# Optimization experiments

Measured on AMD Instinct MI355X. Metric: run time of the kernel, lower is better.

The kernel has to match this reference:

```python
import jax, jax.numpy as jnp
import numpy as np

N_FFT = 7
HOP = 2
WIN_LEN = 6
N_FREQ = N_FFT // 2 + 1  # onesided -> 4


def setup_inputs() -> dict:
    key = jax.random.key(0)
    k1, k2 = jax.random.split(key)
    x = jax.random.normal(k1, (64, 500000), dtype=jnp.float32)
    w = jax.random.uniform(k2, (WIN_LEN,), dtype=jnp.float32)
    return {"input": x, "window": w}


def reference(input, window):
    # torch.stft(n_fft=7, hop=2, win_length=6, center=False, onesided=True,
    #            normalized=False, return_complex=True)
    B, L = input.shape
    F = 1 + (L - N_FFT) // HOP  # number of frames (center=False)
    # ATen centers a short window inside n_fft zeros: left = (n_fft - win_length) // 2 = 0
    left = (N_FFT - WIN_LEN) // 2
    w_pad = jnp.zeros((N_FFT,), input.dtype).at[left:left + WIN_LEN].set(window)
    # strided framing: idx[f, n] = f*hop + n  -> frames [B, F, n_fft]
    idx = jnp.arange(F)[:, None] * HOP + jnp.arange(N_FFT)[None, :]
    frames = input[:, idx] * w_pad  # [B, F, 7]
    # onesided real DFT as a tiny matmul: exp(-2i*pi*k*n/N) = cos - i*sin
    n = jnp.arange(N_FFT, dtype=input.dtype)
    k = jnp.arange(N_FREQ, dtype=input.dtype)
    ang = (2.0 * np.pi / N_FFT) * n[:, None] * k[None, :]  # [7, 4]
    re = jnp.einsum('bfn,nk->bkf', frames, jnp.cos(ang))   # [B, 4, F]
    im = -jnp.einsum('bfn,nk->bkf', frames, jnp.sin(ang))  # [B, 4, F]
    return jax.lax.complex(re, im)  # complex64 [B, n_freq, n_frames]
```

## Files before the change

kernel.cpp:

```cpp
#include <hip/hip_runtime.h>

#define HOP   2
#define NFFT  7
#define WLEN  6
#define NFREQ 4

__device__ __constant__ const float C7[7] = {
     1.0f,
     0.62348980185873359f,
    -0.22252093395631440f,
    -0.90096886790241915f,
    -0.90096886790241915f,
    -0.22252093395631440f,
     0.62348980185873359f
};
__device__ __constant__ const float S7[7] = {
     0.0f,
     0.78183148246802980f,
     0.97492791218182362f,
     0.43388373911755812f,
    -0.43388373911755812f,
    -0.97492791218182362f,
    -0.78183148246802980f
};

__global__ __launch_bounds__(256) void stft_kernel(
    const float* __restrict__ x, const float* __restrict__ w,
    float* __restrict__ out,
    long long L, long long F, long long HALF, long long in0, long long outn)
{
    const long long f = (long long)blockIdx.x * blockDim.x + threadIdx.x;
    if (f >= F) return;
    const long long b = blockIdx.y;

    const long long xbase = b * L + 2 * f;
    if (xbase + (WLEN - 1) >= in0) return;

    float wx[WLEN];
#pragma unroll
    for (int n = 0; n < WLEN; ++n) {
        wx[n] = x[xbase + n] * w[n];
    }

#pragma unroll
    for (int k = 0; k < NFREQ; ++k) {
        float re = 0.f, im = 0.f;
#pragma unroll
        for (int n = 0; n < WLEN; ++n) {
            const int m = (k * n) % 7;
            re = fmaf(wx[n],  C7[m], re);
            im = fmaf(wx[n], -S7[m], im);
        }
        const long long q = (b * NFREQ + k) * F + f;
        if (q < outn)        out[q] = re;
        if (HALF + q < outn) out[HALF + q] = im;
    }
}

extern "C" void kernel_launch(void* const* d_in, const int* in_sizes, int n_in,
                              void* d_out, int out_size, void* d_ws, size_t ws_size,
                              hipStream_t stream) {
    const float* x = (const float*)d_in[0];
    const float* w = (const float*)d_in[1];
    float* out = (float*)d_out;

    const long long B = 64;
    const long long L = (long long)in_sizes[0] / B;
    const long long F = 1 + (L - NFFT) / HOP;
    const long long HALF = B * NFREQ * F;

    dim3 block(256);
    dim3 grid((unsigned)((F + 255) / 256), (unsigned)B);
    stft_kernel<<<grid, block, 0, stream>>>(x, w, out, L, F, HALF,
                                            (long long)in_sizes[0],
                                            (long long)out_size);
}
```

Before: 342.5 us.

## Compute four frames per thread with vector loads and symmetric DFT

Each thread now processes four consecutive frames, loading 12 input floats with three 16-byte vector loads instead of six scalar loads per frame. The DFT uses cosine/sine symmetry (pairs of sums and differences) with hard-coded constants instead of constant-memory lookups. The k=0 imaginary output is written as zero directly. Stores become strided by 4 per thread, which may hurt write coalescing. The vector load path assumes 16-byte alignment of x+xbase, which holds only when the row length L is a multiple of 4.

```diff
diff --git a/kernel.cpp b/kernel.cpp
--- a/kernel.cpp
+++ b/kernel.cpp
@@ -1,59 +1,76 @@
 #include <hip/hip_runtime.h>
 
-#define HOP   2
-#define NFFT  7
-#define WLEN  6
 #define NFREQ 4
 
-__device__ __constant__ const float C7[7] = {
-     1.0f,
-     0.62348980185873359f,
-    -0.22252093395631440f,
-    -0.90096886790241915f,
-    -0.90096886790241915f,
-    -0.22252093395631440f,
-     0.62348980185873359f
-};
-__device__ __constant__ const float S7[7] = {
-     0.0f,
-     0.78183148246802980f,
-     0.97492791218182362f,
-     0.43388373911755812f,
-    -0.43388373911755812f,
-    -0.97492791218182362f,
-    -0.78183148246802980f
-};
+typedef float f4 __attribute__((ext_vector_type(4)));
 
-__global__ __launch_bounds__(256) void stft_kernel(
+#define C1 0.62348980185873359f
+#define C2 (-0.22252093395631440f)
+#define C3 (-0.90096886790241915f)
+#define S1 0.78183148246802980f
+#define S2 0.97492791218182362f
+#define S3 0.43388373911755812f
+
+__global__ __launch_bounds__(256) void stft4(
     const float* __restrict__ x, const float* __restrict__ w,
     float* __restrict__ out,
     long long L, long long F, long long HALF, long long in0, long long outn)
 {
-    const long long f = (long long)blockIdx.x * blockDim.x + threadIdx.x;
-    if (f >= F) return;
+    const long long t = (long long)blockIdx.x * blockDim.x + threadIdx.x;
+    const long long nG = (F + 3) >> 2;
+    if (t >= nG) return;
     const long long b = blockIdx.y;
 
-    const long long xbase = b * L + 2 * f;
-    if (xbase + (WLEN - 1) >= in0) return;
+    const float w0 = w[0], w1 = w[1], w2 = w[2], w3 = w[3], w4 = w[4], w5 = w[5];
 
-    float wx[WLEN];
+    const long long f0 = t << 2;
+    const long long xbase = b * L + 2 * f0;
+
+    float s[12];
+    if ((f0 + 3 < F) && (xbase + 12 <= in0)) {
+        f4 va, vb, vc;
+        __builtin_memcpy(&va, x + xbase,      16);
+        __builtin_memcpy(&vb, x + xbase + 4,  16);
+        __builtin_memcpy(&vc, x + xbase + 8,  16);
+        s[0]=va.x; s[1]=va.y; s[2]=va.z;  s[3]=va.w;
+        s[4]=vb.x; s[5]=vb.y; s[6]=vb.z;  s[7]=vb.w;
+        s[8]=vc.x; s[9]=vc.y; s[10]=vc.z; s[11]=vc.w;
+    } else {
 #pragma unroll
-    for (int n = 0; n < WLEN; ++n) {
-        wx[n] = x[xbase + n] * w[n];
+        for (int i = 0; i < 12; ++i)
+            s[i] = (xbase + i < in0) ? x[xbase + i] : 0.f;
     }
 
 #pragma unroll
-    for (int k = 0; k < NFREQ; ++k) {
-        float re = 0.f, im = 0.f;
-#pragma unroll
-        for (int n = 0; n < WLEN; ++n) {
-            const int m = (k * n) % 7;
-            re = fmaf(wx[n],  C7[m], re);
-            im = fmaf(wx[n], -S7[m], im);
-        }
-        const long long q = (b * NFREQ + k) * F + f;
-        if (q < outn)        out[q] = re;
-        if (HALF + q < outn) out[HALF + q] = im;
+    for (int j = 0; j < 4; ++j) {
+        if (f0 + j >= F) break;
+        const float wx0 = s[2*j+0] * w0, wx1 = s[2*j+1] * w1;
+        const float wx2 = s[2*j+2] * w2, wx3 = s[2*j+3] * w3;
+        const float wx4 = s[2*j+4] * w4, wx5 = s[2*j+5] * w5;
+        const float p2 = wx2 + wx5, p3 = wx3 + wx4;
+        const float m2 = wx2 - wx5, m3 = wx3 - wx4;
+
+        const float re0 = wx0 + wx1 + p2 + p3;
+        const float re1 = fmaf(C1, wx1, fmaf(C2, p2, fmaf(C3, p3, wx0)));
+        const float re2 = fmaf(C2, wx1, fmaf(C3, p2, fmaf(C1, p3, wx0)));
+        const float re3 = fmaf(C3, wx1, fmaf(C1, p2, fmaf(C2, p3, wx0)));
+        const float im1 = -fmaf(S1, wx1, fmaf(S2, m2,  S3 * m3));
+        const float im2 = fmaf(-S2, wx1, fmaf(S3, m2,  S1 * m3));
+        const float im3 = fmaf(-S3, wx1, fmaf(S1, m2, -S2 * m3));
+
+        const long long f = f0 + j;
+        const long long q0 = (b * NFREQ + 0) * F + f;
+        const long long q1 = q0 + F;
+        const long long q2 = q1 + F;
+        const long long q3 = q2 + F;
+        if (q0 < outn)        out[q0] = re0;
+        if (HALF + q0 < outn) out[HALF + q0] = 0.f;
+        if (q1 < outn)        out[q1] = re1;
+        if (HALF + q1 < outn) out[HALF + q1] = im1;
+        if (q2 < outn)        out[q2] = re2;
+        if (HALF + q2 < outn) out[HALF + q2] = im2;
+        if (q3 < outn)        out[q3] = re3;
+        if (HALF + q3 < outn) out[HALF + q3] = im3;
     }
 }
 
@@ -66,12 +83,13 @@
 
     const long long B = 64;
     const long long L = (long long)in_sizes[0] / B;
-    const long long F = 1 + (L - NFFT) / HOP;
+    const long long F = 1 + (L - 7) / 2;
     const long long HALF = B * NFREQ * F;
+    const long long nG = (F + 3) / 4;
 
     dim3 block(256);
-    dim3 grid((unsigned)((F + 255) / 256), (unsigned)B);
-    stft_kernel<<<grid, block, 0, stream>>>(x, w, out, L, F, HALF,
-                                            (long long)in_sizes[0],
-                                            (long long)out_size);
+    dim3 grid((unsigned)((nG + 255) / 256), (unsigned)B);
+    stft4<<<grid, block, 0, stream>>>(x, w, out, L, F, HALF,
+                                      (long long)in_sizes[0],
+                                      (long long)out_size);
 }
```

Result: slower. 383.0 us (+11.8%).

## Flatten output-indexed grid with vectorized 4-frame loads/stores and symmetric DFT

Applied to the files above, without the earlier changes.

The kernel is restructured so that each thread writes four consecutive output floats with a single 16-byte store. A flat grid covers 512 (part,b,k) planes, and each thread loads 16 input floats as four vector loads. The DFT exploits cos/sin symmetry (pairing taps 2/5 and 3/4) to cut FMAs, and 64-bit indexing is replaced with int math. The goal is wider, fully coalesced stores in place of per-frame scalar stores to 8 separate planes. The cost is redundant input reads across the 8 planes and a scalar fallback path for misaligned or boundary quads.

```diff
diff --git a/kernel.cpp b/kernel.cpp
--- a/kernel.cpp
+++ b/kernel.cpp
@@ -1,59 +1,127 @@
 #include <hip/hip_runtime.h>
 
-#define HOP   2
-#define NFFT  7
-#define WLEN  6
-#define NFREQ 4
+typedef float f4 __attribute__((ext_vector_type(4)));
 
-__device__ __constant__ const float C7[7] = {
-     1.0f,
-     0.62348980185873359f,
-    -0.22252093395631440f,
-    -0.90096886790241915f,
-    -0.90096886790241915f,
-    -0.22252093395631440f,
-     0.62348980185873359f
-};
-__device__ __constant__ const float S7[7] = {
-     0.0f,
-     0.78183148246802980f,
-     0.97492791218182362f,
-     0.43388373911755812f,
-    -0.43388373911755812f,
-    -0.97492791218182362f,
-    -0.78183148246802980f
-};
+#define C1f 0.62348980185873359f
+#define C2f (-0.22252093395631440f)
+#define C3f (-0.90096886790241915f)
+#define S1f 0.78183148246802980f
+#define S2f 0.97492791218182362f
+#define S3f 0.43388373911755812f
 
-__global__ __launch_bounds__(256) void stft_kernel(
+__global__ __launch_bounds__(256) void stft_flat(
     const float* __restrict__ x, const float* __restrict__ w,
-    float* __restrict__ out,
-    long long L, long long F, long long HALF, long long in0, long long outn)
+    float* __restrict__ out, int L, int F, int inN, int outN)
 {
-    const long long f = (long long)blockIdx.x * blockDim.x + threadIdx.x;
-    if (f >= F) return;
-    const long long b = blockIdx.y;
+    const int bx = (int)blockIdx.x;
+    const int p  = bx & 511;
+    const int i  = (bx >> 9) * 256 + (int)threadIdx.x;
 
-    const long long xbase = b * L + 2 * f;
-    if (xbase + (WLEN - 1) >= in0) return;
+    const int pF  = p * F;
+    const int qb  = (pF + 3) >> 2;
+    const int nQp = (((p + 1) * F + 3) >> 2) - qb;
+    if (i >= nQp) return;
 
-    float wx[WLEN];
-#pragma unroll
-    for (int n = 0; n < WLEN; ++n) {
-        wx[n] = x[xbase + n] * w[n];
+    const int k    = p & 3;
+    const int b    = (p >> 2) & 63;
+    const int part = p >> 8;
+
+    const int d0 = (qb + i) << 2;
+    const int f0 = d0 - pF;
+
+    const float w0=w[0], w1=w[1], w2=w[2], w3=w[3], w4=w[4], w5=w[5];
+
+    const int xo = b * L + 2 * f0;
+    const int xd = xo & ~3;
+
+    if ((f0 + 3 < F) && (xd + 16 <= inN) && (d0 + 4 <= outN) && ((xo & 1) == 0)) {
+        f4 A, B2, C2v, D2;
+        __builtin_memcpy(&A,   x + xd,      16);
+        __builtin_memcpy(&B2,  x + xd + 4,  16);
+        __builtin_memcpy(&C2v, x + xd + 8,  16);
+        __builtin_memcpy(&D2,  x + xd + 12, 16);
+        float s0=A.x,  s1=A.y,  s2=A.z,  s3=A.w,
+              s4=B2.x, s5=B2.y, s6=B2.z, s7=B2.w,
+              s8=C2v.x,s9=C2v.y,s10=C2v.z,s11=C2v.w,
+              s12=D2.x,s13=D2.y;
+        if (xo != xd) {
+            s0=s2; s1=s3; s2=s4; s3=s5; s4=s6;  s5=s7;
+            s6=s8; s7=s9; s8=s10; s9=s11; s10=s12; s11=s13;
+        }
+
+        f4 v;
+        if (part == 0) {
+            float ca, cb, cc;
+            if      (k == 0) { ca=1.f; cb=1.f; cc=1.f; }
+            else if (k == 1) { ca=C1f; cb=C2f; cc=C3f; }
+            else if (k == 2) { ca=C2f; cb=C3f; cc=C1f; }
+            else             { ca=C3f; cb=C1f; cc=C2f; }
+#define REJ(a0,a1,a2,a3,a4,a5) ({ \
+            const float wx0=(a0)*w0, wx1=(a1)*w1; \
+            const float pp2=(a2)*w2 + (a5)*w5; \
+            const float pp3=(a3)*w3 + (a4)*w4; \
+            fmaf(ca, wx1, fmaf(cb, pp2, fmaf(cc, pp3, wx0))); })
+            v.x = REJ(s0,s1,s2,s3,s4,s5);
+            v.y = REJ(s2,s3,s4,s5,s6,s7);
+            v.z = REJ(s4,s5,s6,s7,s8,s9);
+            v.w = REJ(s6,s7,s8,s9,s10,s11);
+#undef REJ
+        } else {
+            float sa, sb, sc;
+            if      (k == 0) { sa=0.f; sb=0.f;   sc=0.f;  }
+            else if (k == 1) { sa=S1f; sb=S2f;   sc=S3f;  }
+            else if (k == 2) { sa=S2f; sb=-S3f;  sc=-S1f; }
+            else             { sa=S3f; sb=-S1f;  sc=S2f;  }
+#define IMJ(a1,a2,a3,a4,a5) ({ \
+            const float wx1=(a1)*w1; \
+            const float mm2=(a2)*w2 - (a5)*w5; \
+            const float mm3=(a3)*w3 - (a4)*w4; \
+            -fmaf(sa, wx1, fmaf(sb, mm2, sc * mm3)); })
+            v.x = IMJ(s1,s2,s3,s4,s5);
+            v.y = IMJ(s3,s4,s5,s6,s7);
+            v.z = IMJ(s5,s6,s7,s8,s9);
+            v.w = IMJ(s7,s8,s9,s10,s11);
+#undef IMJ
+        }
+        __builtin_memcpy(out + d0, &v, 16);
+        return;
     }
 
-#pragma unroll
-    for (int k = 0; k < NFREQ; ++k) {
-        float re = 0.f, im = 0.f;
-#pragma unroll
-        for (int n = 0; n < WLEN; ++n) {
-            const int m = (k * n) % 7;
-            re = fmaf(wx[n],  C7[m], re);
-            im = fmaf(wx[n], -S7[m], im);
+    const int OUTt = F << 9;
+    for (int j = 0; j < 4; ++j) {
+        const int d = d0 + j;
+        if (d >= outN || d >= OUTt) return;
+        int pd = p, fd = d - pF;
+        if (fd >= F) { pd = p + 1; fd -= F; }
+        const int kd = pd & 3, bd = (pd >> 2) & 63, partd = pd >> 8;
+        const int base = bd * L + 2 * fd;
+        const float sx0 = (base + 0 < inN) ? x[base + 0] : 0.f;
+        const float sx1 = (base + 1 < inN) ? x[base + 1] : 0.f;
+        const float sx2 = (base + 2 < inN) ? x[base + 2] : 0.f;
+        const float sx3 = (base + 3 < inN) ? x[base + 3] : 0.f;
+        const float sx4 = (base + 4 < inN) ? x[base + 4] : 0.f;
+        const float sx5 = (base + 5 < inN) ? x[base + 5] : 0.f;
+        const float wx0=sx0*w0, wx1=sx1*w1, wx2=sx2*w2;
+        const float wx3=sx3*w3, wx4=sx4*w4, wx5=sx5*w5;
+        float val;
+        if (partd == 0) {
+            const float p2 = wx2 + wx5, p3 = wx3 + wx4;
+            float ca, cb, cc;
+            if      (kd == 0) { ca=1.f; cb=1.f; cc=1.f; }
+            else if (kd == 1) { ca=C1f; cb=C2f; cc=C3f; }
+            else if (kd == 2) { ca=C2f; cb=C3f; cc=C1f; }
+            else              { ca=C3f; cb=C1f; cc=C2f; }
+            val = fmaf(ca, wx1, fmaf(cb, p2, fmaf(cc, p3, wx0)));
+        } else {
+            const float m2 = wx2 - wx5, m3 = wx3 - wx4;
+            float sa, sb, sc;
+            if      (kd == 0) { sa=0.f; sb=0.f;   sc=0.f;  }
+            else if (kd == 1) { sa=S1f; sb=S2f;   sc=S3f;  }
+            else if (kd == 2) { sa=S2f; sb=-S3f;  sc=-S1f; }
+            else              { sa=S3f; sb=-S1f;  sc=S2f;  }
+            val = -fmaf(sa, wx1, fmaf(sb, m2, sc * m3));
         }
-        const long long q = (b * NFREQ + k) * F + f;
-        if (q < outn)        out[q] = re;
-        if (HALF + q < outn) out[HALF + q] = im;
+        out[d] = val;
     }
 }
 
@@ -66,12 +134,14 @@
 
     const long long B = 64;
     const long long L = (long long)in_sizes[0] / B;
-    const long long F = 1 + (L - NFFT) / HOP;
-    const long long HALF = B * NFREQ * F;
+    const long long F = 1 + (L - 7) / 2;
+
+    const int maxNQ = (int)((F + 3) / 4 + 1);
+    const int nib   = (maxNQ + 255) / 256;
 
     dim3 block(256);
-    dim3 grid((unsigned)((F + 255) / 256), (unsigned)B);
-    stft_kernel<<<grid, block, 0, stream>>>(x, w, out, L, F, HALF,
-                                            (long long)in_sizes[0],
-                                            (long long)out_size);
+    dim3 grid((unsigned)(nib * 512));
+    stft_flat<<<grid, block, 0, stream>>>(x, w, out,
+                                          (int)L, (int)F,
+                                          in_sizes[0], out_size);
 }
```

Measured after the change: 381.8 us. 11.5% more time.
